# Kernel tuning notes

Hardware: AMD Instinct MI355X
Metric: run time of the kernel (lower is better)

## Reference

```python
import jax, jax.numpy as jnp
import numpy as np

B, C, E, H = 2, 2048, 1024, 16
HD = E // H


def setup_inputs() -> dict:
    key = jax.random.key(0)
    k_x, k_len, k_w1, k_b1, k_w2, k_b2 = jax.random.split(key, 6)
    x = jax.random.normal(k_x, (B, C, E), dtype=jnp.float32)
    # pad_mask: True where token is valid; random valid lengths in [C//2, C]
    lengths = jax.random.randint(k_len, (B,), C // 2, C + 1)
    pad_mask = jnp.arange(C)[None, :] < lengths[:, None]  # [B, C] bool
    s1 = 1.0 / np.sqrt(E)
    w_qkv = jax.random.uniform(k_w1, (3 * E, E), jnp.float32, -s1, s1)  # torch Linear weight [out,in]
    b_qkv = jax.random.uniform(k_b1, (3 * E,), jnp.float32, -s1, s1)
    w_out = jax.random.uniform(k_w2, (E, E), jnp.float32, -s1, s1)
    b_out = jax.random.uniform(k_b2, (E,), jnp.float32, -s1, s1)
    return {"x": x, "pad_mask": pad_mask, "w_qkv": w_qkv, "b_qkv": b_qkv,
            "w_out": w_out, "b_out": b_out}


def reference(x, pad_mask, w_qkv, b_qkv, w_out, b_out):
    b, c, e = x.shape
    qkv = x @ w_qkv.T + b_qkv                      # [B, C, 3E]
    qkv = qkv.reshape(b, c, 3, H, HD)
    qkv = jnp.transpose(qkv, (2, 0, 3, 1, 4))      # [3, B, H, C, HD]
    q, k, v = qkv[0], qkv[1], qkv[2]
    scores = jnp.einsum('bhqd,bhkd->bhqk', q, k) / np.sqrt(HD)  # [B,H,C,C]
    causal = jnp.tril(jnp.ones((c, c), dtype=bool))
    scores = jnp.where(causal[None, None, :, :], scores, -1e9)
    scores = jnp.where(pad_mask[:, None, None, :], scores, -1e9)
    attn = jax.nn.softmax(scores, axis=-1)
    out = jnp.einsum('bhqk,bhkd->bhqd', attn, v)   # [B,H,C,HD]
    out = jnp.transpose(out, (0, 2, 1, 3)).reshape(b, c, e)
    return out @ w_out.T + b_out
```

## Files before the change

### kernel.cpp

```cpp
#include <hip/hip_runtime.h>
#include <cstdint>
#include <cstddef>

typedef short short8 __attribute__((ext_vector_type(8)));
typedef float f32x4 __attribute__((ext_vector_type(4)));

#define NB 2
#define NC 2048
#define NE 1024
#define NH 16
#define ND 64
#define QSZ (NB*NH*NC*ND)

typedef const __attribute__((address_space(1))) void GV;
typedef __attribute__((address_space(3))) void LV;

__device__ __forceinline__ unsigned short f32_to_bf16(float f) {
    union { float f; unsigned u; } v; v.f = f;
    return (unsigned short)((v.u + 0x7fffu + ((v.u >> 16) & 1u)) >> 16);
}

__global__ __launch_bounds__(256) void fused_cast_kernel(
    const float* __restrict__ x, const float* __restrict__ wqkv,
    const float* __restrict__ wout, const void* __restrict__ pad,
    unsigned short* __restrict__ x_bf, unsigned short* __restrict__ wqkv_bf,
    unsigned short* __restrict__ wout_bf, int* __restrict__ lengths)
{
    const int bid = blockIdx.x, tid = threadIdx.x;
    if (bid < 8192) {
        const float* src; unsigned short* dst; int i;
        if (bid < 4096)      { src = x;    dst = x_bf;    i = bid*256 + tid; }
        else if (bid < 7168) { src = wqkv; dst = wqkv_bf; i = (bid-4096)*256 + tid; }
        else                 { src = wout; dst = wout_bf; i = (bid-7168)*256 + tid; }
        float4 v = ((const float4*)src)[i];
        ushort4 o;
        o.x = f32_to_bf16(v.x); o.y = f32_to_bf16(v.y);
        o.z = f32_to_bf16(v.z); o.w = f32_to_bf16(v.w);
        ((ushort4*)dst)[i] = o;
    } else {
        const int b = bid - 8192;
        unsigned w0 = ((const unsigned*)pad)[0];
        int cnt = 0;
        for (int i = tid; i < NC; i += 256) {
            int idx = b*NC + i;
            bool valid;
            if (w0 == 1u)               valid = ((const int*)pad)[idx] != 0;
            else if (w0 == 0x3f800000u) valid = ((const float*)pad)[idx] != 0.0f;
            else                        valid = ((const unsigned char*)pad)[idx] != 0;
            cnt += valid ? 1 : 0;
        }
        cnt += __shfl_xor(cnt, 1);  cnt += __shfl_xor(cnt, 2);
        cnt += __shfl_xor(cnt, 4);  cnt += __shfl_xor(cnt, 8);
        cnt += __shfl_xor(cnt, 16); cnt += __shfl_xor(cnt, 32);
        __shared__ int ws_[4];
        if ((tid & 63) == 0) ws_[tid >> 6] = cnt;
        __syncthreads();
        if (tid == 0) lengths[b] = ws_[0] + ws_[1] + ws_[2] + ws_[3];
    }
}

template<int EPI, int TM, int WPE>
__global__ __launch_bounds__(256, WPE) void gemm_bt_kernel(
    const unsigned short* __restrict__ A,
    const unsigned short* __restrict__ Bw,
    const float* __restrict__ bias,
    float* __restrict__ outF,
    unsigned short* __restrict__ outQ,
    int M, int N, int K)
{
    constexpr int NF = (TM == 128) ? 4 : 2;
    constexpr int WCW = 16 * NF;
    __shared__ unsigned short As[TM*64];
    __shared__ unsigned short Bs[128*64];
    const int tid = threadIdx.x;
    const int w = tid >> 6, lane = tid & 63;
    const int wr = (TM == 128) ? (w >> 1) : 0;
    const int wc = (TM == 128) ? (w & 1) : w;
    const int g = lane >> 4, lr = lane & 15;
    const int nbx = N >> 7, nwg = gridDim.x;
    const int id = blockIdx.x;
    const int swz = (id & 7) * (nwg >> 3) + (id >> 3);
    const int mBase = (swz / nbx) * TM, nBase = (swz % nbx) * 128;

    f32x4 acc[4][NF];
#pragma unroll
    for (int m = 0; m < 4; ++m)
#pragma unroll
        for (int n = 0; n < NF; ++n) acc[m][n] = (f32x4){0.f, 0.f, 0.f, 0.f};

    constexpr int AJ = TM / 32;
    int srow[4], scol[4]; unsigned ldso[4];
#pragma unroll
    for (int j = 0; j < 4; ++j) {
        int o = ((j*4 + w) << 10) + lane*16;
        int row = o >> 7;
        int chunk = ((o >> 4) & 7) ^ (row & 7);
        srow[j] = row; scol[j] = chunk * 8; ldso[j] = (unsigned)((j*4 + w) << 10);
    }

    const int nk = K >> 6;
    for (int kt = 0; kt < nk; ++kt) {
        const int k0 = kt << 6;
#pragma unroll
        for (int j = 0; j < AJ; ++j) {
            const unsigned short* ga = A + (size_t)(mBase + srow[j])*K + (k0 + scol[j]);
            __builtin_amdgcn_global_load_lds((GV*)ga, (LV*)((char*)As + ldso[j]), 16, 0, 0);
        }
#pragma unroll
        for (int j = 0; j < 4; ++j) {
            const unsigned short* gb = Bw + (size_t)(nBase + srow[j])*K + (k0 + scol[j]);
            __builtin_amdgcn_global_load_lds((GV*)gb, (LV*)((char*)Bs + ldso[j]), 16, 0, 0);
        }
        __syncthreads();
#pragma unroll
        for (int ks = 0; ks < 2; ++ks) {
            short8 af[4], bf[NF];
#pragma unroll
            for (int m = 0; m < 4; ++m) {
                int row = wr*64 + m*16 + lr;
                int chunk = (ks*4 + g) ^ (row & 7);
                af[m] = *(const short8*)((const char*)As + row*128 + chunk*16);
            }
#pragma unroll
            for (int n = 0; n < NF; ++n) {
                int row = wc*WCW + n*16 + lr;
                int chunk = (ks*4 + g) ^ (row & 7);
                bf[n] = *(const short8*)((const char*)Bs + row*128 + chunk*16);
            }
#pragma unroll
            for (int m = 0; m < 4; ++m)
#pragma unroll
                for (int n = 0; n < NF; ++n)
                    acc[m][n] = __builtin_amdgcn_mfma_f32_16x16x32_bf16(af[m], bf[n], acc[m][n], 0, 0, 0);
        }
        __syncthreads();
    }

    if constexpr (EPI == 0) {
#pragma unroll
        for (int n = 0; n < NF; ++n) {
            int col = nBase + wc*WCW + n*16 + lr;
            float bv = bias[col];
#pragma unroll
            for (int m = 0; m < 4; ++m) {
                int rowb = mBase + wr*64 + m*16 + 4*g;
#pragma unroll
                for (int r = 0; r < 4; ++r)
                    outF[(size_t)(rowb + r)*N + col] = acc[m][n][r] + bv;
            }
        }
    } else {
        if (nBase >= 2048) {
#pragma unroll
            for (int n = 0; n < NF; ++n) {
                int col = nBase + wc*WCW + n*16 + lr;
                float bv = bias[col];
                int hh = (col >> 6) & 15, d = col & 63;
#pragma unroll
                for (int m = 0; m < 4; ++m) {
                    int rowb = mBase + wr*64 + m*16 + 4*g;
                    int bb = rowb >> 11, c = rowb & 2047;
                    int cp = (c & ~63) | ((m >> 1) << 5) | (g << 3) | ((m & 1) << 2);
                    size_t base = (((size_t)((4 + bb)*16 + hh))*64 + d)*2048 + cp;
                    float v0 = acc[m][n][0] + bv, v1 = acc[m][n][1] + bv;
                    float v2 = acc[m][n][2] + bv, v3 = acc[m][n][3] + bv;
                    unsigned w0, w1;
                    asm("v_cvt_pk_bf16_f32 %0, %1, %2" : "=v"(w0) : "v"(v0), "v"(v1));
                    asm("v_cvt_pk_bf16_f32 %0, %1, %2" : "=v"(w1) : "v"(v2), "v"(v3));
                    union { unsigned u[2]; uint2 v; } pk2; pk2.u[0] = w0; pk2.u[1] = w1;
                    *(uint2*)(outQ + base) = pk2.v;
                }
            }
        } else {
#pragma unroll
            for (int n = 0; n < NF; ++n) {
                int col = nBase + wc*WCW + n*16 + lr;
                float bv = bias[col];
                int t = col >> 10, hh = (col >> 6) & 15, d = col & 63;
                float qscale = (t == 0) ? 0.1803368801f : 1.0f;
#pragma unroll
                for (int m = 0; m < 4; ++m) {
                    int rowb = mBase + wr*64 + m*16 + 4*g;
#pragma unroll
                    for (int r = 0; r < 4; ++r) {
                        int row = rowb + r;
                        int bb = row >> 11, c = row & 2047;
                        unsigned short bf16v = f32_to_bf16((acc[m][n][r] + bv) * qscale);
                        size_t idx = ((((size_t)(t*2 + bb))*16 + hh)*2048 + c)*64 + d;
                        outQ[idx] = bf16v;
                    }
                }
            }
        }
    }
}

__global__ __launch_bounds__(256, 4) void attn_kernel(
    const unsigned short* __restrict__ qkv,
    const int* __restrict__ lengths,
    unsigned short* __restrict__ ctx)
{
    __shared__ unsigned short Kt[2][64*64];
    __shared__ unsigned short Vt[2][64*64];
    const int bh = blockIdx.x;
    const int b = bh >> 4, h = bh & 15;
    const int y = blockIdx.y;
    const int qb = (y < 8) ? 31 - y : (y < 16) ? y - 8 : (y < 24) ? 39 - y : y - 16;
    const int q0 = qb * 64;
    const int len = lengths[b];
    const int nt = min(qb + 1, (len + 63) >> 6);
    const int tid = threadIdx.x, w = tid >> 6, lane = tid & 63;
    const int g = lane >> 4, lr = lane & 15;
    const unsigned short* qp = qkv +          ((size_t)(b*NH + h))*NC*ND;
    const unsigned short* kp = qkv + QSZ    + ((size_t)(b*NH + h))*NC*ND;
    const unsigned short* vp = qkv + 2*QSZ  + ((size_t)(b*NH + h))*ND*NC;
    const int qw0 = q0 + w*16;

    short8 aq[2];
#pragma unroll
    for (int ks = 0; ks < 2; ++ks)
        aq[ks] = *(const short8*)(qp + (size_t)(qw0 + lr)*ND + ks*32 + 8*g);

    f32x4 oa[4];
#pragma unroll
    for (int n = 0; n < 4; ++n) oa[n] = (f32x4){0.f, 0.f, 0.f, 0.f};
    f32x4 acc_l = (f32x4){0.f, 0.f, 0.f, 0.f};
    union { unsigned u[4]; short8 s; } ones;
    ones.u[0] = ones.u[1] = ones.u[2] = ones.u[3] = 0x3F803F80u;

    int srw[2], sck[2]; unsigned ldso[2];
#pragma unroll
    for (int j = 0; j < 2; ++j) {
        int o = ((j*4 + w) << 10) + lane*16;
        int row = o >> 7;
        int chunk = ((o >> 4) & 7) ^ (row & 7);
        srw[j] = row; sck[j] = chunk * 8; ldso[j] = (unsigned)((j*4 + w) << 10);
    }

#define STAGE(T, BUF) do {                                                        \
    int k0s = (T) << 6;                                                           \
    _Pragma("unroll")                                                             \
    for (int j = 0; j < 2; ++j) {                                                 \
        const unsigned short* gk = kp + (size_t)(k0s + srw[j])*ND + sck[j];       \
        const unsigned short* gv = vp + (size_t)srw[j]*NC + k0s + sck[j];         \
        __builtin_amdgcn_global_load_lds((GV*)gk, (LV*)((char*)Kt[BUF] + ldso[j]), 16, 0, 0); \
        __builtin_amdgcn_global_load_lds((GV*)gv, (LV*)((char*)Vt[BUF] + ldso[j]), 16, 0, 0); \
    } } while (0)

    STAGE(0, 0);
    __syncthreads();

#pragma unroll 2
    for (int t = 0; t < nt; ++t) {
        if (t + 1 < nt) STAGE(t + 1, (t + 1) & 1);
        const char* Kb = (const char*)Kt[t & 1];
        const char* Vb = (const char*)Vt[t & 1];
        const int k0 = t << 6;

        f32x4 sa[4];
#pragma unroll
        for (int a = 0; a < 4; ++a) sa[a] = (f32x4){0.f, 0.f, 0.f, 0.f};
        __builtin_amdgcn_s_setprio(1);
#pragma unroll
        for (int ks = 0; ks < 2; ++ks) {
#pragma unroll
            for (int a = 0; a < 4; ++a) {
                int row = a*16 + lr;
                int chunk = (ks*4 + g) ^ (row & 7);
                short8 ak = *(const short8*)(Kb + row*128 + chunk*16);
                sa[a] = __builtin_amdgcn_mfma_f32_16x16x32_bf16(ak, aq[ks], sa[a], 0, 0, 0);
            }
        }
        __builtin_amdgcn_s_setprio(0);

        float p[4][4];
        const bool edge = (t == nt - 1);
        if (!edge) {
#pragma unroll
            for (int a = 0; a < 4; ++a)
#pragma unroll
                for (int r = 0; r < 4; ++r)
                    p[a][r] = exp2f(sa[a][r]);
        } else {
            const int qg = qw0 + lr;
            const int kb0 = k0 + 4*g;
#pragma unroll
            for (int a = 0; a < 4; ++a)
#pragma unroll
                for (int r = 0; r < 4; ++r) {
                    int key = kb0 + 16*a + r;
                    p[a][r] = (key <= qg && key < len) ? exp2f(sa[a][r]) : 0.f;
                }
        }

        unsigned pw0, pw1, pw2, pw3, pw4, pw5, pw6, pw7;
        asm("v_cvt_pk_bf16_f32 %0, %1, %2" : "=v"(pw0) : "v"(p[0][0]), "v"(p[0][1]));
        asm("v_cvt_pk_bf16_f32 %0, %1, %2" : "=v"(pw1) : "v"(p[0][2]), "v"(p[0][3]));
        asm("v_cvt_pk_bf16_f32 %0, %1, %2" : "=v"(pw2) : "v"(p[1][0]), "v"(p[1][1]));
        asm("v_cvt_pk_bf16_f32 %0, %1, %2" : "=v"(pw3) : "v"(p[1][2]), "v"(p[1][3]));
        asm("v_cvt_pk_bf16_f32 %0, %1, %2" : "=v"(pw4) : "v"(p[2][0]), "v"(p[2][1]));
        asm("v_cvt_pk_bf16_f32 %0, %1, %2" : "=v"(pw5) : "v"(p[2][2]), "v"(p[2][3]));
        asm("v_cvt_pk_bf16_f32 %0, %1, %2" : "=v"(pw6) : "v"(p[3][0]), "v"(p[3][1]));
        asm("v_cvt_pk_bf16_f32 %0, %1, %2" : "=v"(pw7) : "v"(p[3][2]), "v"(p[3][3]));
        union { unsigned u[4]; short8 s; } pu0, pu1;
        pu0.u[0] = pw0; pu0.u[1] = pw1; pu0.u[2] = pw2; pu0.u[3] = pw3;
        pu1.u[0] = pw4; pu1.u[1] = pw5; pu1.u[2] = pw6; pu1.u[3] = pw7;

        __builtin_amdgcn_s_setprio(1);
#pragma unroll
        for (int ks = 0; ks < 2; ++ks) {
            short8 pa = ks ? pu1.s : pu0.s;
            acc_l = __builtin_amdgcn_mfma_f32_16x16x32_bf16(pa, ones.s, acc_l, 0, 0, 0);
#pragma unroll
            for (int n = 0; n < 4; ++n) {
                int row = n*16 + lr;
                int chunk = (ks*4 + g) ^ (row & 7);
                short8 bv = *(const short8*)(Vb + row*128 + chunk*16);
                oa[n] = __builtin_amdgcn_mfma_f32_16x16x32_bf16(pa, bv, oa[n], 0, 0, 0);
            }
        }
        __builtin_amdgcn_s_setprio(0);

        __syncthreads();
    }
#undef STAGE

#pragma unroll
    for (int r = 0; r < 4; ++r) {
        float inv = 1.0f / acc_l[r];
        int qg = qw0 + 4*g + r;
        size_t base = ((size_t)b*NC + qg)*NE + h*ND;
#pragma unroll
        for (int n = 0; n < 4; ++n)
            ctx[base + n*16 + lr] = f32_to_bf16(oa[n][r] * inv);
    }
}

extern "C" void kernel_launch(void* const* d_in, const int* in_sizes, int n_in,
                              void* d_out, int out_size, void* d_ws, size_t ws_size,
                              hipStream_t stream)
{
    const float* x    = (const float*)d_in[0];
    const void*  pad  = d_in[1];
    const float* wqkv = (const float*)d_in[2];
    const float* bqkv = (const float*)d_in[3];
    const float* wout = (const float*)d_in[4];
    const float* bout = (const float*)d_in[5];
    float* out = (float*)d_out;

    unsigned short* x_bf    = (unsigned short*)d_ws;
    unsigned short* wqkv_bf = x_bf    + 4194304;
    unsigned short* wout_bf = wqkv_bf + 3145728;
    unsigned short* qkv     = wout_bf + 1048576;
    unsigned short* ctx     = qkv     + 12582912;
    int*            lens    = (int*)(ctx + 4194304);

    fused_cast_kernel<<<8194, 256, 0, stream>>>(x, wqkv, wout, pad,
                                                x_bf, wqkv_bf, wout_bf, lens);

    gemm_bt_kernel<1,128,3><<<768, 256, 0, stream>>>(x_bf, wqkv_bf, bqkv,
                                                     nullptr, qkv, 4096, 3072, 1024);
    attn_kernel<<<dim3(32, 32), 256, 0, stream>>>(qkv, lens, ctx);
    gemm_bt_kernel<0,64,2><<<512, 256, 0, stream>>>(ctx, wout_bf, bout,
                                                    out, nullptr, 4096, 1024, 1024);
}
```

Measured before the change: 90.82 us.

## Add dedicated 256x192-tile double-buffered QKV GEMM with interleaved load/MFMA schedule

Replaces the generic 128-row GEMM for the QKV projection with a specialised 512-thread kernel that uses 256x192 output tiles, double-buffered LDS fed by global_load_lds, and a schedule that splits each K-step into four MFMA phases with loads issued between them and raised wave priority during MFMA. Block indices are swizzled to improve L2 reuse, and the epilogue keeps the transposed V layout and Q scaling expected by the attention kernel. The aim is more data reuse per tile and better overlap of memory with matrix cores. In exchange it launches only 256 blocks, uses large LDS and register footprints, and relies on hand-tuned waitcnt counts.

```diff
diff --git a/kernel.cpp b/kernel.cpp
--- a/kernel.cpp
+++ b/kernel.cpp
@@ -59,6 +59,156 @@
     }
 }
 
+__global__ __launch_bounds__(512, 2) void gemm_qkv_kernel(
+    const unsigned short* __restrict__ A,
+    const unsigned short* __restrict__ Bw,
+    const float* __restrict__ bias,
+    unsigned short* __restrict__ outQ)
+{
+    constexpr int K = 1024;
+    __shared__ unsigned short As[2][256*64];
+    __shared__ unsigned short Bs[2][192*64];
+    const int tid = threadIdx.x;
+    const int w = tid >> 6, lane = tid & 63;
+    const int wr = w >> 2, wc = w & 3;
+    const int g = lane >> 4, lr = lane & 15;
+    const int id = blockIdx.x;
+    const int swz = (id & 7) * 32 + (id >> 3);
+    const int mBase = (swz >> 4) * 256, nBase = (swz & 15) * 192;
+
+    f32x4 acc[8][3];
+#pragma unroll
+    for (int m = 0; m < 8; ++m)
+#pragma unroll
+        for (int n = 0; n < 3; ++n) acc[m][n] = (f32x4){0.f, 0.f, 0.f, 0.f};
+
+    int srw[4], sck[4]; unsigned ldso[4];
+#pragma unroll
+    for (int j = 0; j < 4; ++j) {
+        int o = ((j*8 + w) << 10) + lane*16;
+        int row = o >> 7;
+        int chunk = ((o >> 4) & 7) ^ (row & 7);
+        srw[j] = row; sck[j] = chunk * 8; ldso[j] = (unsigned)((j*8 + w) << 10);
+    }
+    const unsigned short* Abase = A  + (size_t)mBase * K;
+    const unsigned short* Bbase = Bw + (size_t)nBase * K;
+
+#define QISS_B(kt, buf) do { _Pragma("unroll")                                    \
+    for (int j = 0; j < 3; ++j) {                                                 \
+        const unsigned short* gb = Bbase + (size_t)srw[j]*K + ((kt)<<6) + sck[j]; \
+        __builtin_amdgcn_global_load_lds((GV*)gb, (LV*)((char*)Bs[buf] + ldso[j]), 16, 0, 0); \
+    } } while (0)
+#define QISS_A2(kt, buf, j0, j1) do {                                             \
+        const unsigned short* g0 = Abase + (size_t)srw[j0]*K + ((kt)<<6) + sck[j0]; \
+        __builtin_amdgcn_global_load_lds((GV*)g0, (LV*)((char*)As[buf] + ldso[j0]), 16, 0, 0); \
+        const unsigned short* g1 = Abase + (size_t)srw[j1]*K + ((kt)<<6) + sck[j1]; \
+        __builtin_amdgcn_global_load_lds((GV*)g1, (LV*)((char*)As[buf] + ldso[j1]), 16, 0, 0); \
+    } while (0)
+#define QRD_B(buf, ks) do { _Pragma("unroll")                                     \
+    for (int n = 0; n < 3; ++n) {                                                 \
+        int row = wc*48 + n*16 + lr;                                              \
+        int chunk = ((ks)*4 + g) ^ (row & 7);                                     \
+        bf[n] = *(const short8*)((const char*)Bs[buf] + row*128 + chunk*16);      \
+    } } while (0)
+#define QRD_A(buf, ks, mh) do { _Pragma("unroll")                                 \
+    for (int m = 0; m < 4; ++m) {                                                 \
+        int row = wr*128 + (mh)*64 + m*16 + lr;                                   \
+        int chunk = ((ks)*4 + g) ^ (row & 7);                                     \
+        af[m] = *(const short8*)((const char*)As[buf] + row*128 + chunk*16);      \
+    } } while (0)
+#define QMM(mh) do { _Pragma("unroll")                                            \
+    for (int m = 0; m < 4; ++m) { _Pragma("unroll")                               \
+    for (int n = 0; n < 3; ++n)                                                   \
+        acc[(mh)*4+m][n] = __builtin_amdgcn_mfma_f32_16x16x32_bf16(af[m], bf[n], acc[(mh)*4+m][n], 0, 0, 0); \
+    } } while (0)
+#define QBAR __builtin_amdgcn_s_barrier()
+
+    short8 af[4], bf[3];
+
+    QISS_B(0, 0); QISS_A2(0, 0, 0, 2); QISS_A2(0, 0, 1, 3);
+    asm volatile("s_waitcnt vmcnt(2)" ::: "memory");
+    QBAR;
+
+    for (int kt = 0; kt < 15; ++kt) {
+        const int b = kt & 1, b1 = b ^ 1;
+        QRD_B(b, 0); QRD_A(b, 0, 0);
+        QISS_B(kt + 1, b1);
+        asm volatile("s_waitcnt vmcnt(3)" ::: "memory");
+        QBAR;
+        __builtin_amdgcn_s_setprio(1); QMM(0); __builtin_amdgcn_s_setprio(0);
+        QBAR;
+        QRD_A(b, 0, 1);
+        QISS_A2(kt + 1, b1, 0, 2);
+        QBAR;
+        __builtin_amdgcn_s_setprio(1); QMM(1); __builtin_amdgcn_s_setprio(0);
+        QBAR;
+        QRD_B(b, 1); QRD_A(b, 1, 0);
+        QISS_A2(kt + 1, b1, 1, 3);
+        QBAR;
+        __builtin_amdgcn_s_setprio(1); QMM(0); __builtin_amdgcn_s_setprio(0);
+        QBAR;
+        QRD_A(b, 1, 1);
+        asm volatile("s_waitcnt vmcnt(2)" ::: "memory");
+        QBAR;
+        __builtin_amdgcn_s_setprio(1); QMM(1); __builtin_amdgcn_s_setprio(0);
+        QBAR;
+    }
+    QRD_B(1, 0); QRD_A(1, 0, 0);
+    asm volatile("s_waitcnt vmcnt(0)" ::: "memory");
+    QBAR;
+    QMM(0);
+    QRD_A(1, 0, 1); QMM(1);
+    QRD_B(1, 1); QRD_A(1, 1, 0); QMM(0);
+    QRD_A(1, 1, 1); QMM(1);
+
+#undef QISS_B
+#undef QISS_A2
+#undef QRD_B
+#undef QRD_A
+#undef QMM
+#undef QBAR
+
+#pragma unroll
+    for (int n = 0; n < 3; ++n) {
+        const int colb = nBase + wc*48 + n*16;
+        const int col = colb + lr;
+        const float bv = bias[col];
+        if (colb >= 2048) {
+            const int hh = (col >> 6) & 15, d = col & 63;
+#pragma unroll
+            for (int m = 0; m < 8; ++m) {
+                int rowb = mBase + wr*128 + m*16 + 4*g;
+                int bb = rowb >> 11, c = rowb & 2047;
+                int mq = m & 3;
+                int cp = (c & ~63) | ((mq >> 1) << 5) | (g << 3) | ((mq & 1) << 2);
+                size_t base = (((size_t)((4 + bb)*16 + hh))*64 + d)*2048 + cp;
+                float v0 = acc[m][n][0] + bv, v1 = acc[m][n][1] + bv;
+                float v2 = acc[m][n][2] + bv, v3 = acc[m][n][3] + bv;
+                unsigned w0, w1;
+                asm("v_cvt_pk_bf16_f32 %0, %1, %2" : "=v"(w0) : "v"(v0), "v"(v1));
+                asm("v_cvt_pk_bf16_f32 %0, %1, %2" : "=v"(w1) : "v"(v2), "v"(v3));
+                union { unsigned u[2]; uint2 v; } pk2; pk2.u[0] = w0; pk2.u[1] = w1;
+                *(uint2*)(outQ + base) = pk2.v;
+            }
+        } else {
+            const int t = col >> 10, hh = (col >> 6) & 15, d = col & 63;
+            const float qscale = (t == 0) ? 0.1803368801f : 1.0f;
+#pragma unroll
+            for (int m = 0; m < 8; ++m) {
+                int rowb = mBase + wr*128 + m*16 + 4*g;
+#pragma unroll
+                for (int r = 0; r < 4; ++r) {
+                    int row = rowb + r;
+                    int bb = row >> 11, c = row & 2047;
+                    unsigned short bf16v = f32_to_bf16((acc[m][n][r] + bv) * qscale);
+                    size_t idx = ((((size_t)(t*2 + bb))*16 + hh)*2048 + c)*64 + d;
+                    outQ[idx] = bf16v;
+                }
+            }
+        }
+    }
+}
+
 template<int EPI, int TM, int WPE>
 __global__ __launch_bounds__(256, WPE) void gemm_bt_kernel(
     const unsigned short* __restrict__ A,
@@ -358,8 +508,7 @@
     fused_cast_kernel<<<8194, 256, 0, stream>>>(x, wqkv, wout, pad,
                                                 x_bf, wqkv_bf, wout_bf, lens);
 
-    gemm_bt_kernel<1,128,3><<<768, 256, 0, stream>>>(x_bf, wqkv_bf, bqkv,
-                                                     nullptr, qkv, 4096, 3072, 1024);
+    gemm_qkv_kernel<<<256, 512, 0, stream>>>(x_bf, wqkv_bf, bqkv, qkv);
     attn_kernel<<<dim3(32, 32), 256, 0, stream>>>(qkv, lens, ctx);
     gemm_bt_kernel<0,64,2><<<512, 256, 0, stream>>>(ctx, wout_bf, bout,
                                                     out, nullptr, 4096, 1024, 1024);
```

New measurement: 94.36 us. 1.04x slower.
